# Kernel optimization log

Hardware: AMD Instinct MI355X
Metric: run time of the kernel (lower is better)

## Reference

```python
import jax, jax.numpy as jnp
import numpy as np

B, D, H = 32768, 688, 4
DH = D // H          # 172 head dim (d_model // h, overrides ctor d_k)
MH = 128             # mlp hidden
EPS = 1e-5
SCALE = 1.0 / float(np.sqrt(DH))


def _ln(x, g, b):
    m = jnp.mean(x, -1, keepdims=True)
    v = jnp.var(x, -1, keepdims=True)  # biased var, matches torch LayerNorm
    return (x - m) / jnp.sqrt(v + EPS) * g + b


def setup_inputs() -> dict:
    key = jax.random.key(0)
    ks = jax.random.split(key, 16)
    w = lambda k, o, i: jax.random.normal(k, (o, i), jnp.float32) * 0.001  # init.normal_(std=0.001)
    z = lambda n: jnp.zeros((n,), jnp.float32)
    o = lambda n: jnp.ones((n,), jnp.float32)
    return dict(
        x=jax.random.normal(ks[0], (B, D), jnp.float32),
        x2=jax.random.normal(ks[1], (B, D), jnp.float32),
        Wq_v=w(ks[2], D, D), bq_v=z(D),
        Wk_v=w(ks[3], D, D), bk_v=z(D),
        Wv_v=w(ks[4], D, D), bv_v=z(D),
        Wq_i=w(ks[5], D, D), bq_i=z(D),
        Wk_i=w(ks[6], D, D), bk_i=z(D),
        Wv_i=w(ks[7], D, D), bv_i=z(D),
        Wo_v=w(ks[8], D, D), bo_v=z(D),
        Wo_i=w(ks[9], D, D), bo_i=z(D),
        ln1_g=o(D), ln1_b=z(D), ln2_g=o(D), ln2_b=z(D),
        ln3_g=o(D), ln3_b=z(D), ln4_g=o(D), ln4_b=z(D),
        m1v_W=w(ks[10], MH, D), m1v_b=z(MH),
        m2v_W=w(ks[11], D, MH), m2v_b=z(D),
        m1i_W=w(ks[12], MH, D), m1i_b=z(MH),
        m2i_W=w(ks[13], D, MH), m2i_b=z(D),
        coef=o(8),  # LearnableCoefficient 1..8, all init to 1.0
    )


def reference(x, x2,
              Wq_v, bq_v, Wk_v, bk_v, Wv_v, bv_v,
              Wq_i, bq_i, Wk_i, bk_i, Wv_i, bv_i,
              Wo_v, bo_v, Wo_i, bo_i,
              ln1_g, ln1_b, ln2_g, ln2_b, ln3_g, ln3_b, ln4_g, ln4_b,
              m1v_W, m1v_b, m2v_W, m2v_b, m1i_W, m1i_b, m2i_W, m2i_b,
              coef):
    rgb = _ln(x, ln1_g, ln1_b)
    ir = _ln(x2, ln2_g, ln2_b)
    proj = lambda t, W, b: (t @ W.T + b).reshape(-1, H, DH)  # (B, h, d_k)
    q_vis, k_vis, v_vis = proj(rgb, Wq_v, bq_v), proj(rgb, Wk_v, bk_v), proj(rgb, Wv_v, bv_v)
    q_ir, k_ir, v_ir = proj(ir, Wq_i, bq_i), proj(ir, Wk_i, bk_i), proj(ir, Wv_i, bv_i)
    # cross attention over heads: scores are (B, h, h)
    att_vis = jax.nn.softmax(jnp.einsum('bhd,bgd->bhg', q_ir, k_vis) * SCALE, -1)
    att_ir = jax.nn.softmax(jnp.einsum('bhd,bgd->bhg', q_vis, k_ir) * SCALE, -1)
    out_vis = jnp.einsum('bhg,bgd->bhd', att_vis, v_vis).reshape(-1, D) @ Wo_v.T + bo_v
    out_ir = jnp.einsum('bhg,bgd->bhd', att_ir, v_ir).reshape(-1, D) @ Wo_i.T + bo_i
    out_vis = coef[0] * x + coef[1] * out_vis
    out_ir = coef[2] * x2 + coef[3] * out_ir
    mv = jax.nn.gelu(_ln(out_vis, ln3_g, ln3_b) @ m1v_W.T + m1v_b, approximate=False) @ m2v_W.T + m2v_b
    mi = jax.nn.gelu(_ln(out_ir, ln4_g, ln4_b) @ m1i_W.T + m1i_b, approximate=False) @ m2i_W.T + m2i_b
    out_vis = coef[4] * out_vis + coef[5] * mv
    out_ir = coef[6] * out_ir + coef[7] * mi
    return out_vis, out_ir
```

## Files before the change

### kernel.cpp

```cpp
#include <hip/hip_runtime.h>
#include <cmath>


#define B_ROWS 32768
#define D_DIM  688
#define DP     704
#define DH_DIM 172
#define MH_DIM 128

typedef unsigned short ushort_t;
typedef __attribute__((ext_vector_type(8))) __bf16 bf16x8;
typedef __attribute__((ext_vector_type(4))) float  f32x4;

__device__ __forceinline__ float b2f(ushort_t u) {
    return __builtin_bit_cast(float, (unsigned int)u << 16);
}
__device__ __forceinline__ ushort_t f2bf(float f) {
    unsigned int u = __builtin_bit_cast(unsigned int, f);
    u += 0x7FFFu + ((u >> 16) & 1u);
    return (ushort_t)(u >> 16);
}

__device__ __forceinline__ void gl2lds16(const ushort_t* g, ushort_t* l) {
    __builtin_amdgcn_global_load_lds(
        (const __attribute__((address_space(1))) unsigned int*)g,
        (__attribute__((address_space(3))) unsigned int*)l, 16, 0, 0);
}

struct CvtJobs {
    const float* src[12];
    ushort_t*    dst[12];
    int O[12], Opad[12], Kin[12], Kpad[12];
    int bstart[13];
};

__global__ __launch_bounds__(256)
void cvt_all(CvtJobs jobs)
{
    int b = blockIdx.x;
    int j = 0;
    while (b >= jobs.bstart[j + 1]) ++j;
    const int t = (b - jobs.bstart[j]) * 256 + threadIdx.x;
    const int Kpad = jobs.Kpad[j];
    const int Kin  = jobs.Kin[j];
    const int cpr  = Kpad >> 3;
    if (t >= jobs.Opad[j] * cpr) return;
    const int o = t / cpr;
    const int c = t - o * cpr;
    unsigned int p0 = 0, p1 = 0, p2 = 0, p3 = 0;
    if (o < jobs.O[j] && (c * 8 + 8) <= Kin) {
        const float* s = jobs.src[j] + (size_t)o * Kin + c * 8;
        float4 f0 = reinterpret_cast<const float4*>(s)[0];
        float4 f1 = reinterpret_cast<const float4*>(s)[1];
        p0 = f2bf(f0.x) | ((unsigned int)f2bf(f0.y) << 16);
        p1 = f2bf(f0.z) | ((unsigned int)f2bf(f0.w) << 16);
        p2 = f2bf(f1.x) | ((unsigned int)f2bf(f1.y) << 16);
        p3 = f2bf(f1.z) | ((unsigned int)f2bf(f1.w) << 16);
    }
    *reinterpret_cast<uint4*>(jobs.dst[j] + (size_t)o * Kpad + c * 8) =
        make_uint4(p0, p1, p2, p3);
}

__global__ __launch_bounds__(256)
void pack_bias(const float* __restrict__ a0, const float* __restrict__ a1,
               const float* __restrict__ a2, const float* __restrict__ b0,
               const float* __restrict__ b1, const float* __restrict__ b2,
               float* __restrict__ dv, float* __restrict__ di)
{
    int t = blockIdx.x * 256 + threadIdx.x;
    if (t >= 2064) return;
    float v, w;
    if (t < 688)       { v = a0[t];        w = b0[t]; }
    else if (t < 1376) { v = a1[t - 688];  w = b1[t - 688]; }
    else               { v = a2[t - 1376]; w = b2[t - 1376]; }
    dv[t] = v; di[t] = w;
}

__global__ __launch_bounds__(256)
void ln_kernel(const float* __restrict__ Xv, const float* __restrict__ Xi,
               const float* __restrict__ gv, const float* __restrict__ bv,
               const float* __restrict__ gi, const float* __restrict__ bi,
               ushort_t* __restrict__ Yv, ushort_t* __restrict__ Yi)
{
    const int lane = threadIdx.x & 63;
    const int wave = threadIdx.x >> 6;
    const long w = (long)blockIdx.x * 4 + wave;
    const float* X; const float* g; const float* b; ushort_t* Y; long r;
    if (w < B_ROWS) { X = Xv; g = gv; b = bv; Y = Yv; r = w; }
    else            { X = Xi; g = gi; b = bi; Y = Yi; r = w - B_ROWS; }

    const float4* row = reinterpret_cast<const float4*>(X + r * D_DIM);
    float4 v0 = row[lane];
    float4 v1 = row[lane + 64];
    float4 v2 = make_float4(0.f, 0.f, 0.f, 0.f);
    if (lane < 44) v2 = row[lane + 128];

    float s  = v0.x + v0.y + v0.z + v0.w + v1.x + v1.y + v1.z + v1.w
             + v2.x + v2.y + v2.z + v2.w;
    float s2 = v0.x*v0.x + v0.y*v0.y + v0.z*v0.z + v0.w*v0.w
             + v1.x*v1.x + v1.y*v1.y + v1.z*v1.z + v1.w*v1.w
             + v2.x*v2.x + v2.y*v2.y + v2.z*v2.z + v2.w*v2.w;
#pragma unroll
    for (int m = 32; m; m >>= 1) { s += __shfl_xor(s, m); s2 += __shfl_xor(s2, m); }

    const float mean = s * (1.f / 688.f);
    const float var  = s2 * (1.f / 688.f) - mean * mean;
    const float rstd = rsqrtf(var + 1e-5f);

    const float4* g4 = reinterpret_cast<const float4*>(g);
    const float4* b4 = reinterpret_cast<const float4*>(b);
    ushort4* out4 = reinterpret_cast<ushort4*>(Y + r * DP);

    {
        float4 gg = g4[lane], bb = b4[lane];
        ushort4 o;
        o.x = f2bf((v0.x - mean) * rstd * gg.x + bb.x);
        o.y = f2bf((v0.y - mean) * rstd * gg.y + bb.y);
        o.z = f2bf((v0.z - mean) * rstd * gg.z + bb.z);
        o.w = f2bf((v0.w - mean) * rstd * gg.w + bb.w);
        out4[lane] = o;
    }
    {
        float4 gg = g4[lane + 64], bb = b4[lane + 64];
        ushort4 o;
        o.x = f2bf((v1.x - mean) * rstd * gg.x + bb.x);
        o.y = f2bf((v1.y - mean) * rstd * gg.y + bb.y);
        o.z = f2bf((v1.z - mean) * rstd * gg.z + bb.z);
        o.w = f2bf((v1.w - mean) * rstd * gg.w + bb.w);
        out4[lane + 64] = o;
    }
    if (lane < 44) {
        float4 gg = g4[lane + 128], bb = b4[lane + 128];
        ushort4 o;
        o.x = f2bf((v2.x - mean) * rstd * gg.x + bb.x);
        o.y = f2bf((v2.y - mean) * rstd * gg.y + bb.y);
        o.z = f2bf((v2.z - mean) * rstd * gg.z + bb.z);
        o.w = f2bf((v2.w - mean) * rstd * gg.w + bb.w);
        out4[lane + 128] = o;
    } else if (lane < 48) {
        out4[lane + 128] = make_ushort4(0, 0, 0, 0);
    }
}

template<int MODE>
__global__ __launch_bounds__(512, 1)
void gemm8(const ushort_t* __restrict__ A0, const ushort_t* __restrict__ A1,
           const ushort_t* __restrict__ W0, const ushort_t* __restrict__ W1,
           const float* __restrict__ bias0, const float* __restrict__ bias1,
           ushort_t* __restrict__ out0, ushort_t* __restrict__ out1,
           const float* __restrict__ res0, const float* __restrict__ res1,
           const float* __restrict__ coef, int ca0, int cb0, int ca1, int cb1,
           int NBn, int N, int K, int lda, int ldw, int ldo)
{
    __shared__ __align__(16) ushort_t lds8[65536];

    const int q8 = gridDim.x >> 3;
    const int v  = (blockIdx.x & 7) * q8 + (blockIdx.x >> 3);
    const int nb = v % NBn;
    const int tmp = v / NBn;
    const int mb = tmp & 127;
    const int zz = tmp >> 7;

    const ushort_t* A = zz ? A1 : A0;
    const ushort_t* W = zz ? W1 : W0;
    const float* bias = zz ? bias1 : bias0;
    ushort_t* outp    = zz ? out1 : out0;
    const float* resid = zz ? res1 : res0;
    const int ca = zz ? ca1 : ca0;
    const int cb = zz ? cb1 : cb0;

    const int tid  = threadIdx.x;
    const int lane = tid & 63;
    const int wave = tid >> 6;
    const int wrow = wave >> 2;
    const int wcol = wave & 3;
    const int m0 = mb * 256;
    const int n0 = nb * 256;
    const int rl16 = lane & 15;
    const int q4   = lane >> 4;

    const int r0 = tid >> 3;
    const int u0 = tid & 7;
    const int swz0 = ((u0 ^ (r0 & 7)) * 8);

    f32x4 acc[8][4];
#pragma unroll
    for (int i = 0; i < 8; ++i)
#pragma unroll
        for (int j = 0; j < 4; ++j)
            acc[i][j] = f32x4{0.f, 0.f, 0.f, 0.f};

    const int NT = K >> 6;

#define STAGE8(mat, rbase, ld, kt, hf, tilebase) do {                              \
    const ushort_t* _s = (mat) + (size_t)((rbase) + (hf)*128 + r0) * (ld)          \
                         + (kt)*64 + swz0;                                         \
    gl2lds16(_s,                 (tilebase) + (hf)*8192 + wave*512);               \
    gl2lds16(_s + 64*(size_t)(ld), (tilebase) + (hf)*8192 + 4096 + wave*512);      \
} while (0)

#define RD_A(base, mib, kkv) do {                                                  \
    _Pragma("unroll")                                                              \
    for (int i = 0; i < 4; ++i) {                                                  \
        const int row_ = wrow*128 + ((mib)+i)*16 + rl16;                           \
        const int un_  = (((kkv) >> 3) + q4) ^ (lane & 7);                         \
        af[i] = *reinterpret_cast<const bf16x8*>((base) + row_*64 + un_*8);        \
    } } while (0)

#define RD_B(base, kkv) do {                                                       \
    _Pragma("unroll")                                                              \
    for (int j = 0; j < 4; ++j) {                                                  \
        const int row_ = wcol*64 + j*16 + rl16;                                    \
        const int un_  = (((kkv) >> 3) + q4) ^ (lane & 7);                         \
        bw[j] = *reinterpret_cast<const bf16x8*>((base) + row_*64 + un_*8);        \
    } } while (0)

#define MFMA16(mib) do {                                                           \
    __builtin_amdgcn_s_setprio(1);                                                 \
    _Pragma("unroll")                                                              \
    for (int i = 0; i < 4; ++i)                                                    \
    _Pragma("unroll")                                                              \
    for (int j = 0; j < 4; ++j)                                                    \
        acc[(mib)+i][j] =                                                          \
            __builtin_amdgcn_mfma_f32_16x16x32_bf16(af[i], bw[j], acc[(mib)+i][j], \
                                                    0, 0, 0);                      \
    __builtin_amdgcn_s_setprio(0);                                                 \
} while (0)

    STAGE8(A, m0, lda, 0, 0, lds8);
    STAGE8(A, m0, lda, 0, 1, lds8);
    STAGE8(W, n0, ldw, 0, 0, lds8 + 32768);
    STAGE8(W, n0, ldw, 0, 1, lds8 + 32768);
    STAGE8(W, n0, ldw, 1, 0, lds8 + 49152);
    asm volatile("s_waitcnt vmcnt(2)" ::: "memory");
    __builtin_amdgcn_s_barrier();

    for (int t = 0; t < NT; ++t) {
        ushort_t* const Ab  = lds8 + ((t & 1) * 16384);
        ushort_t* const Bb  = lds8 + 32768 + ((t & 1) * 16384);
        ushort_t* const An  = lds8 + (((t + 1) & 1) * 16384);
        ushort_t* const Bn1 = lds8 + 32768 + (((t + 1) & 1) * 16384);
        ushort_t* const Bn2 = Bb;
        const int tn1 = (t + 1 < NT) ? t + 1 : NT - 1;
        const int tn2 = (t + 2 < NT) ? t + 2 : NT - 1;

        bf16x8 af[4], bw[4];

        RD_A(Ab, 0, 0);
        RD_B(Bb, 0);
        STAGE8(A, m0, lda, tn1, 0, An);
        STAGE8(W, n0, ldw, tn1, 1, Bn1);
        __builtin_amdgcn_s_barrier();
        MFMA16(0);
        __builtin_amdgcn_s_barrier();

        RD_A(Ab, 4, 0);
        STAGE8(A, m0, lda, tn1, 1, An);
        __builtin_amdgcn_s_barrier();
        MFMA16(4);
        __builtin_amdgcn_s_barrier();

        RD_A(Ab, 0, 32);
        RD_B(Bb, 32);
        __builtin_amdgcn_s_barrier();
        MFMA16(0);
        __builtin_amdgcn_s_barrier();

        RD_A(Ab, 4, 32);
        STAGE8(W, n0, ldw, tn2, 0, Bn2);
        asm volatile("s_waitcnt vmcnt(2)" ::: "memory");
        __builtin_amdgcn_s_barrier();
        MFMA16(4);
        __builtin_amdgcn_s_barrier();
    }

    asm volatile("s_waitcnt vmcnt(0)" ::: "memory");
    __builtin_amdgcn_s_barrier();

    ushort_t* const Cl = lds8;
#pragma unroll
    for (int mi = 0; mi < 8; ++mi)
#pragma unroll
        for (int nj = 0; nj < 4; ++nj)
#pragma unroll
            for (int r = 0; r < 4; ++r) {
                const int row  = wrow*128 + mi*16 + q4*4 + r;
                const int colL = wcol*64 + nj*16 + rl16;
                const int blk  = (colL >> 3) ^ (((row >> 2) & 3) << 1);
                Cl[row*256 + blk*8 + (colL & 7)] = f2bf(acc[mi][nj][r]);
            }
    __syncthreads();

    float cA = 0.f, cB = 1.f;
    if constexpr (MODE == 1) { cA = coef[ca]; cB = coef[cb]; }
#pragma unroll
    for (int it2 = 0; it2 < 16; ++it2) {
        const int c   = it2 * 512 + tid;
        const int row = c >> 5;
        const int lb  = c & 31;
        const int gcol = n0 + lb * 8;
        if (gcol >= N) continue;
        const int pb = lb ^ (((row >> 2) & 3) << 1);
        uint4 pv = *reinterpret_cast<const uint4*>(Cl + row*256 + pb*8);
        const ushort_t* pu = (const ushort_t*)&pv;
        float4 b0 = *reinterpret_cast<const float4*>(bias + gcol);
        float4 b1 = *reinterpret_cast<const float4*>(bias + gcol + 4);
        const float bb[8] = {b0.x, b0.y, b0.z, b0.w, b1.x, b1.y, b1.z, b1.w};
        const size_t idx = (size_t)(m0 + row) * ldo + gcol;
        ushort_t o[8];
        if constexpr (MODE == 0) {
#pragma unroll
            for (int k = 0; k < 8; ++k) o[k] = f2bf(b2f(pu[k]) + bb[k]);
        } else {
            const float* rp = resid + idx;
            float4 r0_ = reinterpret_cast<const float4*>(rp)[0];
            float4 r1_ = reinterpret_cast<const float4*>(rp)[1];
            const float rr[8] = {r0_.x, r0_.y, r0_.z, r0_.w, r1_.x, r1_.y, r1_.z, r1_.w};
#pragma unroll
            for (int k = 0; k < 8; ++k)
                o[k] = f2bf(cA * rr[k] + cB * (b2f(pu[k]) + bb[k]));
        }
        *reinterpret_cast<uint4*>(outp + idx) = *reinterpret_cast<uint4*>(o);
    }
#undef STAGE8
#undef RD_A
#undef RD_B
#undef MFMA16
}

template<int MODE>
__global__ __launch_bounds__(256, 4)
void gemm2(const ushort_t* __restrict__ A0, const ushort_t* __restrict__ A1,
           const ushort_t* __restrict__ W0, const ushort_t* __restrict__ W1,
           const float* __restrict__ bias0, const float* __restrict__ bias1,
           void* __restrict__ out0, void* __restrict__ out1,
           const void* __restrict__ res0, const void* __restrict__ res1,
           const float* __restrict__ coef,
           int ca0, int cb0, int ca1, int cb1,
           int NBn, int N, int K, int lda, int ldw, int ldo)
{
    __shared__ __align__(16) ushort_t smem[16384];
    ushort_t* As = smem;
    ushort_t* Bs = smem + 8192;

    const int q  = gridDim.x >> 3;
    const int vb = (blockIdx.x & 7) * q + (blockIdx.x >> 3);
    const int nb = vb % NBn;
    const int tmp = vb / NBn;
    const int mb = tmp & 255;
    const int zz = tmp >> 8;

    const ushort_t* A = zz ? A1 : A0;
    const ushort_t* W = zz ? W1 : W0;
    const float* bias = zz ? bias1 : bias0;
    void* outp        = zz ? out1 : out0;
    const void* resid = zz ? res1 : res0;
    const int ca = zz ? ca1 : ca0;
    const int cb = zz ? cb1 : cb0;

    const int tid  = threadIdx.x;
    const int lane = tid & 63;
    const int wave = tid >> 6;
    const int m0 = mb * 128;
    const int n0 = nb * 128;
    const int wm = (wave >> 1) * 64;
    const int wn = (wave & 1) * 64;

    const int s0 = wave * 128 + lane;
    const int s1 = s0 + 64;
    const ushort_t* pa0 = A + (size_t)(m0 + (s0 >> 2)) * lda + (s0 & 3) * 8;
    const ushort_t* pa1 = A + (size_t)(m0 + (s1 >> 2)) * lda + (s1 & 3) * 8;
    const ushort_t* pb0 = W + (size_t)(n0 + (s0 >> 2)) * ldw + (s0 & 3) * 8;
    const ushort_t* pb1 = W + (size_t)(n0 + (s1 >> 2)) * ldw + (s1 & 3) * 8;

    f32x4 acc[4][4];
#pragma unroll
    for (int i = 0; i < 4; ++i)
#pragma unroll
        for (int j = 0; j < 4; ++j)
            acc[i][j] = f32x4{0.f, 0.f, 0.f, 0.f};

    const int ko = (lane >> 4) * 8;
    const int rl = lane & 15;
    const int nkt = K / 32;

    auto stage = [&](int buf, int kt) {
        const int kof = kt * 32;
        ushort_t* ad = As + buf * 4096 + wave * 1024;
        ushort_t* bd = Bs + buf * 4096 + wave * 1024;
        gl2lds16(pa0 + kof, ad);
        gl2lds16(pa1 + kof, ad + 512);
        gl2lds16(pb0 + kof, bd);
        gl2lds16(pb1 + kof, bd + 512);
    };

    stage(0, 0);
    __syncthreads();

    for (int kt = 0; kt < nkt; ++kt) {
        const int cur = kt & 1;
        if (kt + 1 < nkt) stage(cur ^ 1, kt + 1);

        const ushort_t* Ab = As + cur * 4096;
        const ushort_t* Bb = Bs + cur * 4096;
        bf16x8 af[4], bwv[4];
#pragma unroll
        for (int i = 0; i < 4; ++i) {
            af[i]  = *reinterpret_cast<const bf16x8*>(&Ab[(wm + i * 16 + rl) * 32 + ko]);
            bwv[i] = *reinterpret_cast<const bf16x8*>(&Bb[(wn + i * 16 + rl) * 32 + ko]);
        }
#pragma unroll
        for (int i = 0; i < 4; ++i)
#pragma unroll
            for (int j = 0; j < 4; ++j)
                acc[i][j] = __builtin_amdgcn_mfma_f32_16x16x32_bf16(af[i], bwv[j], acc[i][j], 0, 0, 0);
        __syncthreads();
    }

    float cA = 0.f, cB = 1.f;
    if constexpr (MODE == 3) { cA = coef[ca]; cB = coef[cb]; }
    const int rb = (lane >> 4) * 4;
    const int cl = lane & 15;
    ushort_t* C = smem;
#pragma unroll
    for (int j = 0; j < 4; ++j) {
        const int lcol = wn + j * 16 + cl;
        const int col = n0 + lcol;
        const float bc = (col < N) ? bias[col] : 0.f;
#pragma unroll
        for (int i = 0; i < 4; ++i) {
            const int lrow = wm + i * 16 + rb;
#pragma unroll
            for (int r = 0; r < 4; ++r) {
                float val = acc[i][j][r] + bc;
                C[(lrow + r) * 128 + lcol] = f2bf(val);
            }
        }
    }
    __syncthreads();

#pragma unroll
    for (int p = 0; p < 8; ++p) {
        const int c = tid + p * 256;
        const int lrow = c >> 4;
        const int lcl = (c & 15) * 8;
        const int gcol = n0 + lcl;
        if (gcol >= N) continue;
        const size_t idx = (size_t)(m0 + lrow) * ldo + gcol;
        uint4 pv = *reinterpret_cast<const uint4*>(&C[lrow * 128 + lcl]);
        uint4 rv = *reinterpret_cast<const uint4*>((const ushort_t*)resid + idx);
        const ushort_t* pu = (const ushort_t*)&pv;
        const ushort_t* ru = (const ushort_t*)&rv;
        float o[8];
#pragma unroll
        for (int k = 0; k < 8; ++k)
            o[k] = cA * b2f(ru[k]) + cB * b2f(pu[k]);
        float4* op = reinterpret_cast<float4*>((float*)outp + idx);
        op[0] = make_float4(o[0], o[1], o[2], o[3]);
        op[1] = make_float4(o[4], o[5], o[6], o[7]);
    }
}

__global__ __launch_bounds__(256)
void lnmlp1(const ushort_t* __restrict__ ov0, const ushort_t* __restrict__ ov1,
            const float* __restrict__ g0, const float* __restrict__ b0,
            const float* __restrict__ g1, const float* __restrict__ b1,
            const ushort_t* __restrict__ W10, const ushort_t* __restrict__ W11,
            const float* __restrict__ mb0, const float* __restrict__ mb1,
            ushort_t* __restrict__ out0, ushort_t* __restrict__ out1)
{
    __shared__ __align__(16) ushort_t hraw[64 * 712];
    __shared__ float glds[704];
    __shared__ float blds[704];
    __shared__ float mlds[64];
    __shared__ float rlds[64];

    const int zz = blockIdx.y;
    const ushort_t* ovb = zz ? ov1 : ov0;
    const float* lg = zz ? g1 : g0;
    const float* lb = zz ? b1 : b0;
    const ushort_t* W1 = zz ? W11 : W10;
    const float* mbias = zz ? mb1 : mb0;
    ushort_t* outp = zz ? out1 : out0;

    const int tid  = threadIdx.x;
    const int lane = tid & 63;
    const int wv   = tid >> 6;
    const long r0  = (long)blockIdx.x * 64;

    if (tid < 176) {
        float4 gg = make_float4(0, 0, 0, 0), bb = make_float4(0, 0, 0, 0);
        if (tid < 172) {
            gg = reinterpret_cast<const float4*>(lg)[tid];
            bb = reinterpret_cast<const float4*>(lb)[tid];
        }
        reinterpret_cast<float4*>(glds)[tid] = gg;
        reinterpret_cast<float4*>(blds)[tid] = bb;
    }

#pragma unroll
    for (int it = 0; it < 22; ++it) {
        const int c = it * 256 + tid;
        const int row = c / 88;
        const int u = c - row * 88;
        uint4 vv = make_uint4(0, 0, 0, 0);
        if (u < 86)
            vv = *reinterpret_cast<const uint4*>(ovb + (r0 + row) * 688 + u * 8);
        *reinterpret_cast<uint4*>(&hraw[row * 712 + u * 8]) = vv;
    }
    __syncthreads();

    for (int rr = 0; rr < 16; ++rr) {
        const int row = wv * 16 + rr;
        const ushort_t* hp = &hraw[row * 712];
        ushort4 a0 = *reinterpret_cast<const ushort4*>(hp + lane * 4);
        ushort4 a1 = *reinterpret_cast<const ushort4*>(hp + 256 + lane * 4);
        ushort4 a2 = make_ushort4(0, 0, 0, 0);
        if (lane < 44) a2 = *reinterpret_cast<const ushort4*>(hp + 512 + lane * 4);
        float e[12] = {b2f(a0.x), b2f(a0.y), b2f(a0.z), b2f(a0.w),
                       b2f(a1.x), b2f(a1.y), b2f(a1.z), b2f(a1.w),
                       b2f(a2.x), b2f(a2.y), b2f(a2.z), b2f(a2.w)};
        float s = 0.f, s2 = 0.f;
#pragma unroll
        for (int k = 0; k < 12; ++k) { s += e[k]; s2 += e[k] * e[k]; }
#pragma unroll
        for (int m = 32; m; m >>= 1) { s += __shfl_xor(s, m); s2 += __shfl_xor(s2, m); }
        if (lane == 0) {
            const float mean = s * (1.f / 688.f);
            const float var  = s2 * (1.f / 688.f) - mean * mean;
            mlds[row] = mean;
            rlds[row] = rsqrtf(var + 1e-5f);
        }
    }
    __syncthreads();

#pragma unroll
    for (int it = 0; it < 22; ++it) {
        const int c = it * 256 + tid;
        if (c < 5504) {
            const int row = c / 86;
            const int u = c - row * 86;
            uint4 vv = *reinterpret_cast<const uint4*>(&hraw[row * 712 + u * 8]);
            const float mean = mlds[row], rstd = rlds[row];
            const ushort_t* pe = (const ushort_t*)&vv;
            ushort_t o[8];
#pragma unroll
            for (int k = 0; k < 8; ++k)
                o[k] = f2bf((b2f(pe[k]) - mean) * rstd * glds[u * 8 + k] + blds[u * 8 + k]);
            *reinterpret_cast<uint4*>(&hraw[row * 712 + u * 8]) = *reinterpret_cast<uint4*>(o);
        }
    }
    __syncthreads();

    const int rl16 = lane & 15;
    const int q4   = lane >> 4;
    f32x4 acc[4][2];
#pragma unroll
    for (int i = 0; i < 4; ++i) { acc[i][0] = f32x4{0,0,0,0}; acc[i][1] = f32x4{0,0,0,0}; }

    for (int kt = 0; kt < 11; ++kt) {
#pragma unroll
        for (int kk = 0; kk < 64; kk += 32) {
            bf16x8 af[4], bw[2];
#pragma unroll
            for (int n = 0; n < 2; ++n)
                bw[n] = *reinterpret_cast<const bf16x8*>(
                    W1 + (size_t)(wv * 32 + n * 16 + rl16) * 704 + kt * 64 + kk + q4 * 8);
#pragma unroll
            for (int i = 0; i < 4; ++i)
                af[i] = *reinterpret_cast<const bf16x8*>(
                    &hraw[(i * 16 + rl16) * 712 + kt * 64 + kk + q4 * 8]);
#pragma unroll
            for (int i = 0; i < 4; ++i)
#pragma unroll
                for (int n = 0; n < 2; ++n)
                    acc[i][n] = __builtin_amdgcn_mfma_f32_16x16x32_bf16(
                        af[i], bw[n], acc[i][n], 0, 0, 0);
        }
    }

    const int rb = q4 * 4;
#pragma unroll
    for (int n = 0; n < 2; ++n) {
        const int col = wv * 32 + n * 16 + rl16;
        const float bc = mbias[col];
#pragma unroll
        for (int i = 0; i < 4; ++i)
#pragma unroll
            for (int r = 0; r < 4; ++r) {
                float val = acc[i][n][r] + bc;
                val = 0.5f * val * (1.0f + erff(val * 0.70710678118654752f));
                outp[(r0 + i * 16 + rb + r) * 128 + col] = f2bf(val);
            }
    }
}

__global__ __launch_bounds__(256)
void attn_kernel(const ushort_t* __restrict__ qkv_v, const ushort_t* __restrict__ qkv_i,
                 ushort_t* __restrict__ ctx_v, ushort_t* __restrict__ ctx_i)
{
    const int lane = threadIdx.x & 63;
    const int wave = threadIdx.x >> 6;
    const long r = (long)blockIdx.x * 4 + wave;
    const ushort_t* bv = qkv_v + r * 2064;
    const ushort_t* bi = qkv_i + r * 2064;

    float sv[4][4], si[4][4];
#pragma unroll
    for (int h = 0; h < 4; ++h)
#pragma unroll
        for (int g = 0; g < 4; ++g) { sv[h][g] = 0.f; si[h][g] = 0.f; }

    float vvr[3][4], vir[3][4];
#pragma unroll
    for (int it = 0; it < 3; ++it) {
        const int d = lane + it * 64;
        const bool ok = d < DH_DIM;
        float qv[4], kv[4], qi[4], ki[4];
#pragma unroll
        for (int h = 0; h < 4; ++h) {
            const int o = h * DH_DIM + d;
            qv[h]      = ok ? b2f(bv[o]) : 0.f;
            kv[h]      = ok ? b2f(bv[D_DIM + o]) : 0.f;
            vvr[it][h] = ok ? b2f(bv[2 * D_DIM + o]) : 0.f;
            qi[h]      = ok ? b2f(bi[o]) : 0.f;
            ki[h]      = ok ? b2f(bi[D_DIM + o]) : 0.f;
            vir[it][h] = ok ? b2f(bi[2 * D_DIM + o]) : 0.f;
        }
#pragma unroll
        for (int h = 0; h < 4; ++h)
#pragma unroll
            for (int g = 0; g < 4; ++g) {
                sv[h][g] += qi[h] * kv[g];
                si[h][g] += qv[h] * ki[g];
            }
    }

#pragma unroll
    for (int h = 0; h < 4; ++h)
#pragma unroll
        for (int g = 0; g < 4; ++g) {
            float a = sv[h][g], b = si[h][g];
#pragma unroll
            for (int m = 32; m; m >>= 1) { a += __shfl_xor(a, m); b += __shfl_xor(b, m); }
            sv[h][g] = a; si[h][g] = b;
        }

    const float scale = 0.07624928516630235f;
    float av[4][4], ai[4][4];
#pragma unroll
    for (int h = 0; h < 4; ++h) {
        float m1 = fmaxf(fmaxf(sv[h][0], sv[h][1]), fmaxf(sv[h][2], sv[h][3])) * scale;
        float m2 = fmaxf(fmaxf(si[h][0], si[h][1]), fmaxf(si[h][2], si[h][3])) * scale;
        float d1 = 0.f, d2 = 0.f;
#pragma unroll
        for (int g = 0; g < 4; ++g) {
            av[h][g] = expf(sv[h][g] * scale - m1); d1 += av[h][g];
            ai[h][g] = expf(si[h][g] * scale - m2); d2 += ai[h][g];
        }
        const float r1 = 1.f / d1, r2 = 1.f / d2;
#pragma unroll
        for (int g = 0; g < 4; ++g) { av[h][g] *= r1; ai[h][g] *= r2; }
    }

#pragma unroll
    for (int it = 0; it < 3; ++it) {
        const int d = lane + it * 64;
        if (d < DH_DIM) {
#pragma unroll
            for (int h = 0; h < 4; ++h) {
                float cv = av[h][0] * vvr[it][0] + av[h][1] * vvr[it][1]
                         + av[h][2] * vvr[it][2] + av[h][3] * vvr[it][3];
                float ci = ai[h][0] * vir[it][0] + ai[h][1] * vir[it][1]
                         + ai[h][2] * vir[it][2] + ai[h][3] * vir[it][3];
                ctx_v[r * DP + h * DH_DIM + d] = f2bf(cv);
                ctx_i[r * DP + h * DH_DIM + d] = f2bf(ci);
            }
        }
    }
    if (lane < 16) {
        ctx_v[r * DP + 688 + lane] = 0;
        ctx_i[r * DP + 688 + lane] = 0;
    }
}

extern "C" void kernel_launch(void* const* d_in, const int* in_sizes, int n_in,
                              void* d_out, int out_size, void* d_ws, size_t ws_size,
                              hipStream_t stream)
{
    if (n_in < 35) return;
    const float* x     = (const float*)d_in[0];
    const float* x2    = (const float*)d_in[1];
    const float* Wq_v  = (const float*)d_in[2];
    const float* bq_v  = (const float*)d_in[3];
    const float* Wk_v  = (const float*)d_in[4];
    const float* bk_v  = (const float*)d_in[5];
    const float* Wv_v  = (const float*)d_in[6];
    const float* bv_v  = (const float*)d_in[7];
    const float* Wq_i  = (const float*)d_in[8];
    const float* bq_i  = (const float*)d_in[9];
    const float* Wk_i  = (const float*)d_in[10];
    const float* bk_i  = (const float*)d_in[11];
    const float* Wv_i  = (const float*)d_in[12];
    const float* bv_i  = (const float*)d_in[13];
    const float* Wo_v  = (const float*)d_in[14];
    const float* bo_v  = (const float*)d_in[15];
    const float* Wo_i  = (const float*)d_in[16];
    const float* bo_i  = (const float*)d_in[17];
    const float* ln1_g = (const float*)d_in[18];
    const float* ln1_b = (const float*)d_in[19];
    const float* ln2_g = (const float*)d_in[20];
    const float* ln2_b = (const float*)d_in[21];
    const float* ln3_g = (const float*)d_in[22];
    const float* ln3_b = (const float*)d_in[23];
    const float* ln4_g = (const float*)d_in[24];
    const float* ln4_b = (const float*)d_in[25];
    const float* m1v_W = (const float*)d_in[26];
    const float* m1v_b = (const float*)d_in[27];
    const float* m2v_W = (const float*)d_in[28];
    const float* m2v_b = (const float*)d_in[29];
    const float* m1i_W = (const float*)d_in[30];
    const float* m1i_b = (const float*)d_in[31];
    const float* m2i_W = (const float*)d_in[32];
    const float* m2i_b = (const float*)d_in[33];
    const float* coef  = (const float*)d_in[34];

    const size_t BDP = (size_t)B_ROWS * DP;
    const size_t BD  = (size_t)B_ROWS * D_DIM;

    char* ws = (char*)d_ws;
    size_t off = 0;
    auto give = [&](size_t bytes) {
        char* p = ws + off;
        off += (bytes + 255) & ~(size_t)255;
        return p;
    };
    ushort_t* Wcat_v = (ushort_t*)give(2304ull * DP * 2);
    ushort_t* Wcat_i = (ushort_t*)give(2304ull * DP * 2);
    ushort_t* Wo_vb  = (ushort_t*)give(768ull * DP * 2);
    ushort_t* Wo_ib  = (ushort_t*)give(768ull * DP * 2);
    ushort_t* m1vb   = (ushort_t*)give(128ull * DP * 2);
    ushort_t* m1ib   = (ushort_t*)give(128ull * DP * 2);
    ushort_t* m2vb   = (ushort_t*)give(768ull * 128 * 2);
    ushort_t* m2ib   = (ushort_t*)give(768ull * 128 * 2);
    float*    bcat_v = (float*)give(2064 * 4);
    float*    bcat_i = (float*)give(2064 * 4);
    char* regX = give(BDP * 2 * 2);
    char* regQ = give((size_t)B_ROWS * 2064 * 2 * 2);
    char* regG = give((size_t)B_ROWS * MH_DIM * 2 * 2);
    if (ws_size < off) return;

    ushort_t* xn_v  = (ushort_t*)regX;
    ushort_t* xn_i  = xn_v + BDP;
    ushort_t* ctx_v = xn_v;
    ushort_t* ctx_i = xn_i;
    ushort_t* qkv_v = (ushort_t*)regQ;
    ushort_t* qkv_i = qkv_v + (size_t)B_ROWS * 2064;
    ushort_t* ovb   = (ushort_t*)regQ;
    ushort_t* oib   = ovb + BD;
    ushort_t* g_v   = (ushort_t*)regG;
    ushort_t* g_i   = g_v + (size_t)B_ROWS * MH_DIM;

    float* ov = (float*)d_out;
    float* oi = ov + BD;

    CvtJobs J;
    const float* srcs[12] = {Wq_v, Wk_v, Wv_v, Wq_i, Wk_i, Wv_i,
                             Wo_v, Wo_i, m1v_W, m1i_W, m2v_W, m2i_W};
    ushort_t* dsts[12] = {Wcat_v, Wcat_v + 688 * DP, Wcat_v + 1376 * DP,
                          Wcat_i, Wcat_i + 688 * DP, Wcat_i + 1376 * DP,
                          Wo_vb, Wo_ib, m1vb, m1ib, m2vb, m2ib};
    int Os[12]    = {688, 688, 688, 688, 688, 688, 688, 688, 128, 128, 688, 688};
    int Opads[12] = {688, 688, 928, 688, 688, 928, 768, 768, 128, 128, 768, 768};
    int Kins[12]  = {688, 688, 688, 688, 688, 688, 688, 688, 688, 688, 128, 128};
    int Kpads[12] = {DP, DP, DP, DP, DP, DP, DP, DP, DP, DP, 128, 128};
    int bs = 0;
    for (int j = 0; j < 12; ++j) {
        J.src[j] = srcs[j]; J.dst[j] = dsts[j];
        J.O[j] = Os[j]; J.Opad[j] = Opads[j]; J.Kin[j] = Kins[j]; J.Kpad[j] = Kpads[j];
        J.bstart[j] = bs;
        bs += (Opads[j] * (Kpads[j] >> 3) + 255) / 256;
    }
    J.bstart[12] = bs;
    cvt_all<<<dim3(bs), dim3(256), 0, stream>>>(J);

    pack_bias<<<dim3(9), dim3(256), 0, stream>>>(bq_v, bk_v, bv_v, bq_i, bk_i, bv_i,
                                                 bcat_v, bcat_i);

    ln_kernel<<<dim3(2 * B_ROWS / 4), dim3(256), 0, stream>>>(
        x, x2, ln1_g, ln1_b, ln2_g, ln2_b, xn_v, xn_i);

    gemm8<0><<<dim3(128 * 9 * 2), dim3(512), 0, stream>>>(
        xn_v, xn_i, Wcat_v, Wcat_i, bcat_v, bcat_i, qkv_v, qkv_i,
        nullptr, nullptr, nullptr, 0, 0, 0, 0, 9, 2064, DP, DP, DP, 2064);

    attn_kernel<<<dim3(B_ROWS / 4), dim3(256), 0, stream>>>(qkv_v, qkv_i, ctx_v, ctx_i);

    gemm8<1><<<dim3(128 * 3 * 2), dim3(512), 0, stream>>>(
        ctx_v, ctx_i, Wo_vb, Wo_ib, bo_v, bo_i, ovb, oib,
        x, x2, coef, 0, 1, 2, 3, 3, 688, DP, DP, DP, 688);

    lnmlp1<<<dim3(B_ROWS / 64, 2), dim3(256), 0, stream>>>(
        ovb, oib, ln3_g, ln3_b, ln4_g, ln4_b, m1vb, m1ib, m1v_b, m1i_b, g_v, g_i);

    gemm2<3><<<dim3(256 * 6 * 2), dim3(256), 0, stream>>>(
        g_v, g_i, m2vb, m2ib, m2v_b, m2i_b, ov, oi,
        ovb, oib, coef, 4, 5, 6, 7, 6, 688, 128, 128, 128, 688);
}
```

Baseline: 707.7 us.

## Fuse LayerNorm, MLP up-projection, GELU and down-projection into one kernel

Merges the lnmlp1 kernel and the second MLP GEMM into a single mlp_fused kernel that handles 32 rows per block. The GELU activations stay in shared memory, and the down-projection runs directly from there with the bias and residual combine applied in the epilogue. This removes the global-memory round trip of the hidden activations and one kernel launch. In exchange, W1 and W2 are re-read from global or cache by every block, and the output stores are scalar and strided rather than vectorised.

```diff
diff --git a/kernel.cpp b/kernel.cpp
--- a/kernel.cpp
+++ b/kernel.cpp
@@ -328,165 +328,40 @@
 #undef MFMA16
 }
 
-template<int MODE>
-__global__ __launch_bounds__(256, 4)
-void gemm2(const ushort_t* __restrict__ A0, const ushort_t* __restrict__ A1,
-           const ushort_t* __restrict__ W0, const ushort_t* __restrict__ W1,
-           const float* __restrict__ bias0, const float* __restrict__ bias1,
-           void* __restrict__ out0, void* __restrict__ out1,
-           const void* __restrict__ res0, const void* __restrict__ res1,
-           const float* __restrict__ coef,
-           int ca0, int cb0, int ca1, int cb1,
-           int NBn, int N, int K, int lda, int ldw, int ldo)
+__global__ __launch_bounds__(256)
+void mlp_fused(const ushort_t* __restrict__ ov0, const ushort_t* __restrict__ ov1,
+               const float* __restrict__ g0, const float* __restrict__ b0,
+               const float* __restrict__ g1, const float* __restrict__ b1,
+               const ushort_t* __restrict__ W10, const ushort_t* __restrict__ W11,
+               const float* __restrict__ mb10, const float* __restrict__ mb11,
+               const ushort_t* __restrict__ W20, const ushort_t* __restrict__ W21,
+               const float* __restrict__ mb20, const float* __restrict__ mb21,
+               const float* __restrict__ coef,
+               float* __restrict__ out0, float* __restrict__ out1)
 {
-    __shared__ __align__(16) ushort_t smem[16384];
-    ushort_t* As = smem;
-    ushort_t* Bs = smem + 8192;
-
-    const int q  = gridDim.x >> 3;
-    const int vb = (blockIdx.x & 7) * q + (blockIdx.x >> 3);
-    const int nb = vb % NBn;
-    const int tmp = vb / NBn;
-    const int mb = tmp & 255;
-    const int zz = tmp >> 8;
-
-    const ushort_t* A = zz ? A1 : A0;
-    const ushort_t* W = zz ? W1 : W0;
-    const float* bias = zz ? bias1 : bias0;
-    void* outp        = zz ? out1 : out0;
-    const void* resid = zz ? res1 : res0;
-    const int ca = zz ? ca1 : ca0;
-    const int cb = zz ? cb1 : cb0;
-
-    const int tid  = threadIdx.x;
-    const int lane = tid & 63;
-    const int wave = tid >> 6;
-    const int m0 = mb * 128;
-    const int n0 = nb * 128;
-    const int wm = (wave >> 1) * 64;
-    const int wn = (wave & 1) * 64;
-
-    const int s0 = wave * 128 + lane;
-    const int s1 = s0 + 64;
-    const ushort_t* pa0 = A + (size_t)(m0 + (s0 >> 2)) * lda + (s0 & 3) * 8;
-    const ushort_t* pa1 = A + (size_t)(m0 + (s1 >> 2)) * lda + (s1 & 3) * 8;
-    const ushort_t* pb0 = W + (size_t)(n0 + (s0 >> 2)) * ldw + (s0 & 3) * 8;
-    const ushort_t* pb1 = W + (size_t)(n0 + (s1 >> 2)) * ldw + (s1 & 3) * 8;
-
-    f32x4 acc[4][4];
-#pragma unroll
-    for (int i = 0; i < 4; ++i)
-#pragma unroll
-        for (int j = 0; j < 4; ++j)
-            acc[i][j] = f32x4{0.f, 0.f, 0.f, 0.f};
-
-    const int ko = (lane >> 4) * 8;
-    const int rl = lane & 15;
-    const int nkt = K / 32;
-
-    auto stage = [&](int buf, int kt) {
-        const int kof = kt * 32;
-        ushort_t* ad = As + buf * 4096 + wave * 1024;
-        ushort_t* bd = Bs + buf * 4096 + wave * 1024;
-        gl2lds16(pa0 + kof, ad);
-        gl2lds16(pa1 + kof, ad + 512);
-        gl2lds16(pb0 + kof, bd);
-        gl2lds16(pb1 + kof, bd + 512);
-    };
-
-    stage(0, 0);
-    __syncthreads();
-
-    for (int kt = 0; kt < nkt; ++kt) {
-        const int cur = kt & 1;
-        if (kt + 1 < nkt) stage(cur ^ 1, kt + 1);
-
-        const ushort_t* Ab = As + cur * 4096;
-        const ushort_t* Bb = Bs + cur * 4096;
-        bf16x8 af[4], bwv[4];
-#pragma unroll
-        for (int i = 0; i < 4; ++i) {
-            af[i]  = *reinterpret_cast<const bf16x8*>(&Ab[(wm + i * 16 + rl) * 32 + ko]);
-            bwv[i] = *reinterpret_cast<const bf16x8*>(&Bb[(wn + i * 16 + rl) * 32 + ko]);
-        }
-#pragma unroll
-        for (int i = 0; i < 4; ++i)
-#pragma unroll
-            for (int j = 0; j < 4; ++j)
-                acc[i][j] = __builtin_amdgcn_mfma_f32_16x16x32_bf16(af[i], bwv[j], acc[i][j], 0, 0, 0);
-        __syncthreads();
-    }
-
-    float cA = 0.f, cB = 1.f;
-    if constexpr (MODE == 3) { cA = coef[ca]; cB = coef[cb]; }
-    const int rb = (lane >> 4) * 4;
-    const int cl = lane & 15;
-    ushort_t* C = smem;
-#pragma unroll
-    for (int j = 0; j < 4; ++j) {
-        const int lcol = wn + j * 16 + cl;
-        const int col = n0 + lcol;
-        const float bc = (col < N) ? bias[col] : 0.f;
-#pragma unroll
-        for (int i = 0; i < 4; ++i) {
-            const int lrow = wm + i * 16 + rb;
-#pragma unroll
-            for (int r = 0; r < 4; ++r) {
-                float val = acc[i][j][r] + bc;
-                C[(lrow + r) * 128 + lcol] = f2bf(val);
-            }
-        }
-    }
-    __syncthreads();
-
-#pragma unroll
-    for (int p = 0; p < 8; ++p) {
-        const int c = tid + p * 256;
-        const int lrow = c >> 4;
-        const int lcl = (c & 15) * 8;
-        const int gcol = n0 + lcl;
-        if (gcol >= N) continue;
-        const size_t idx = (size_t)(m0 + lrow) * ldo + gcol;
-        uint4 pv = *reinterpret_cast<const uint4*>(&C[lrow * 128 + lcl]);
-        uint4 rv = *reinterpret_cast<const uint4*>((const ushort_t*)resid + idx);
-        const ushort_t* pu = (const ushort_t*)&pv;
-        const ushort_t* ru = (const ushort_t*)&rv;
-        float o[8];
-#pragma unroll
-        for (int k = 0; k < 8; ++k)
-            o[k] = cA * b2f(ru[k]) + cB * b2f(pu[k]);
-        float4* op = reinterpret_cast<float4*>((float*)outp + idx);
-        op[0] = make_float4(o[0], o[1], o[2], o[3]);
-        op[1] = make_float4(o[4], o[5], o[6], o[7]);
-    }
-}
-
-__global__ __launch_bounds__(256)
-void lnmlp1(const ushort_t* __restrict__ ov0, const ushort_t* __restrict__ ov1,
-            const float* __restrict__ g0, const float* __restrict__ b0,
-            const float* __restrict__ g1, const float* __restrict__ b1,
-            const ushort_t* __restrict__ W10, const ushort_t* __restrict__ W11,
-            const float* __restrict__ mb0, const float* __restrict__ mb1,
-            ushort_t* __restrict__ out0, ushort_t* __restrict__ out1)
-{
-    __shared__ __align__(16) ushort_t hraw[64 * 712];
+    __shared__ __align__(16) ushort_t hraw[32 * 712];
+    __shared__ __align__(16) ushort_t gbuf[32 * 136];
     __shared__ float glds[704];
     __shared__ float blds[704];
-    __shared__ float mlds[64];
-    __shared__ float rlds[64];
+    __shared__ float mlds[32];
+    __shared__ float rlds[32];
 
     const int zz = blockIdx.y;
     const ushort_t* ovb = zz ? ov1 : ov0;
     const float* lg = zz ? g1 : g0;
     const float* lb = zz ? b1 : b0;
     const ushort_t* W1 = zz ? W11 : W10;
-    const float* mbias = zz ? mb1 : mb0;
-    ushort_t* outp = zz ? out1 : out0;
+    const float* mb1 = zz ? mb11 : mb10;
+    const ushort_t* W2 = zz ? W21 : W20;
+    const float* mb2 = zz ? mb21 : mb20;
+    float* outp = zz ? out1 : out0;
+    const float cA = coef[zz ? 6 : 4];
+    const float cB = coef[zz ? 7 : 5];
 
     const int tid  = threadIdx.x;
     const int lane = tid & 63;
     const int wv   = tid >> 6;
-    const long r0  = (long)blockIdx.x * 64;
+    const long r0  = (long)blockIdx.x * 32;
 
     if (tid < 176) {
         float4 gg = make_float4(0, 0, 0, 0), bb = make_float4(0, 0, 0, 0);
@@ -499,7 +374,7 @@
     }
 
 #pragma unroll
-    for (int it = 0; it < 22; ++it) {
+    for (int it = 0; it < 11; ++it) {
         const int c = it * 256 + tid;
         const int row = c / 88;
         const int u = c - row * 88;
@@ -510,8 +385,8 @@
     }
     __syncthreads();
 
-    for (int rr = 0; rr < 16; ++rr) {
-        const int row = wv * 16 + rr;
+    for (int rr = 0; rr < 8; ++rr) {
+        const int row = wv * 8 + rr;
         const ushort_t* hp = &hraw[row * 712];
         ushort4 a0 = *reinterpret_cast<const ushort4*>(hp + lane * 4);
         ushort4 a1 = *reinterpret_cast<const ushort4*>(hp + 256 + lane * 4);
@@ -535,9 +410,9 @@
     __syncthreads();
 
 #pragma unroll
-    for (int it = 0; it < 22; ++it) {
+    for (int it = 0; it < 11; ++it) {
         const int c = it * 256 + tid;
-        if (c < 5504) {
+        if (c < 2752) {
             const int row = c / 86;
             const int u = c - row * 86;
             uint4 vv = *reinterpret_cast<const uint4*>(&hraw[row * 712 + u * 8]);
@@ -554,43 +429,76 @@
 
     const int rl16 = lane & 15;
     const int q4   = lane >> 4;
-    f32x4 acc[4][2];
-#pragma unroll
-    for (int i = 0; i < 4; ++i) { acc[i][0] = f32x4{0,0,0,0}; acc[i][1] = f32x4{0,0,0,0}; }
-
-    for (int kt = 0; kt < 11; ++kt) {
-#pragma unroll
-        for (int kk = 0; kk < 64; kk += 32) {
-            bf16x8 af[4], bw[2];
-#pragma unroll
-            for (int n = 0; n < 2; ++n)
-                bw[n] = *reinterpret_cast<const bf16x8*>(
-                    W1 + (size_t)(wv * 32 + n * 16 + rl16) * 704 + kt * 64 + kk + q4 * 8);
-#pragma unroll
-            for (int i = 0; i < 4; ++i)
-                af[i] = *reinterpret_cast<const bf16x8*>(
-                    &hraw[(i * 16 + rl16) * 712 + kt * 64 + kk + q4 * 8]);
-#pragma unroll
-            for (int i = 0; i < 4; ++i)
+
+    {
+        f32x4 acc[2][2];
+#pragma unroll
+        for (int i = 0; i < 2; ++i) { acc[i][0] = f32x4{0,0,0,0}; acc[i][1] = f32x4{0,0,0,0}; }
+        for (int kt = 0; kt < 11; ++kt) {
+#pragma unroll
+            for (int kk = 0; kk < 64; kk += 32) {
+                bf16x8 af[2], bw[2];
 #pragma unroll
                 for (int n = 0; n < 2; ++n)
-                    acc[i][n] = __builtin_amdgcn_mfma_f32_16x16x32_bf16(
-                        af[i], bw[n], acc[i][n], 0, 0, 0);
-        }
-    }
-
-    const int rb = q4 * 4;
-#pragma unroll
-    for (int n = 0; n < 2; ++n) {
-        const int col = wv * 32 + n * 16 + rl16;
-        const float bc = mbias[col];
-#pragma unroll
-        for (int i = 0; i < 4; ++i)
+                    bw[n] = *reinterpret_cast<const bf16x8*>(
+                        W1 + (size_t)(wv * 32 + n * 16 + rl16) * 704 + kt * 64 + kk + q4 * 8);
+#pragma unroll
+                for (int i = 0; i < 2; ++i)
+                    af[i] = *reinterpret_cast<const bf16x8*>(
+                        &hraw[(i * 16 + rl16) * 712 + kt * 64 + kk + q4 * 8]);
+#pragma unroll
+                for (int i = 0; i < 2; ++i)
+#pragma unroll
+                    for (int n = 0; n < 2; ++n)
+                        acc[i][n] = __builtin_amdgcn_mfma_f32_16x16x32_bf16(
+                            af[i], bw[n], acc[i][n], 0, 0, 0);
+            }
+        }
+        const int rb = q4 * 4;
+#pragma unroll
+        for (int n = 0; n < 2; ++n) {
+            const int col = wv * 32 + n * 16 + rl16;
+            const float bc = mb1[col];
+#pragma unroll
+            for (int i = 0; i < 2; ++i)
+#pragma unroll
+                for (int r = 0; r < 4; ++r) {
+                    float val = acc[i][n][r] + bc;
+                    val = 0.5f * val * (1.0f + erff(val * 0.70710678118654752f));
+                    gbuf[(i * 16 + rb + r) * 136 + col] = f2bf(val);
+                }
+        }
+    }
+    __syncthreads();
+
+    for (int ch = 0; ch < 11; ++ch) {
+        const int col16 = wv * 176 + ch * 16;
+        if (col16 >= 688) continue;
+        f32x4 acc2[2];
+        acc2[0] = f32x4{0, 0, 0, 0};
+        acc2[1] = f32x4{0, 0, 0, 0};
+#pragma unroll
+        for (int kk = 0; kk < 4; ++kk) {
+            bf16x8 bw2 = *reinterpret_cast<const bf16x8*>(
+                W2 + (size_t)(col16 + rl16) * 128 + kk * 32 + q4 * 8);
+            bf16x8 af2[2];
+#pragma unroll
+            for (int i = 0; i < 2; ++i)
+                af2[i] = *reinterpret_cast<const bf16x8*>(
+                    &gbuf[(i * 16 + rl16) * 136 + kk * 32 + q4 * 8]);
+#pragma unroll
+            for (int i = 0; i < 2; ++i)
+                acc2[i] = __builtin_amdgcn_mfma_f32_16x16x32_bf16(af2[i], bw2, acc2[i], 0, 0, 0);
+        }
+        const int col = col16 + rl16;
+        const float bc = mb2[col];
+#pragma unroll
+        for (int i = 0; i < 2; ++i)
 #pragma unroll
             for (int r = 0; r < 4; ++r) {
-                float val = acc[i][n][r] + bc;
-                val = 0.5f * val * (1.0f + erff(val * 0.70710678118654752f));
-                outp[(r0 + i * 16 + rb + r) * 128 + col] = f2bf(val);
+                const long row = r0 + i * 16 + q4 * 4 + r;
+                const float raw = b2f(ovb[row * 688 + col]);
+                outp[row * 688 + col] = cA * raw + cB * (acc2[i][r] + bc);
             }
     }
 }
@@ -747,7 +655,6 @@
     float*    bcat_i = (float*)give(2064 * 4);
     char* regX = give(BDP * 2 * 2);
     char* regQ = give((size_t)B_ROWS * 2064 * 2 * 2);
-    char* regG = give((size_t)B_ROWS * MH_DIM * 2 * 2);
     if (ws_size < off) return;
 
     ushort_t* xn_v  = (ushort_t*)regX;
@@ -758,8 +665,6 @@
     ushort_t* qkv_i = qkv_v + (size_t)B_ROWS * 2064;
     ushort_t* ovb   = (ushort_t*)regQ;
     ushort_t* oib   = ovb + BD;
-    ushort_t* g_v   = (ushort_t*)regG;
-    ushort_t* g_i   = g_v + (size_t)B_ROWS * MH_DIM;
 
     float* ov = (float*)d_out;
     float* oi = ov + BD;
@@ -800,10 +705,8 @@
         ctx_v, ctx_i, Wo_vb, Wo_ib, bo_v, bo_i, ovb, oib,
         x, x2, coef, 0, 1, 2, 3, 3, 688, DP, DP, DP, 688);
 
-    lnmlp1<<<dim3(B_ROWS / 64, 2), dim3(256), 0, stream>>>(
-        ovb, oib, ln3_g, ln3_b, ln4_g, ln4_b, m1vb, m1ib, m1v_b, m1i_b, g_v, g_i);
-
-    gemm2<3><<<dim3(256 * 6 * 2), dim3(256), 0, stream>>>(
-        g_v, g_i, m2vb, m2ib, m2v_b, m2i_b, ov, oi,
-        ovb, oib, coef, 4, 5, 6, 7, 6, 688, 128, 128, 128, 688);
-}
+    mlp_fused<<<dim3(B_ROWS / 32, 2), dim3(256), 0, stream>>>(
+        ovb, oib, ln3_g, ln3_b, ln4_g, ln4_b,
+        m1vb, m1ib, m1v_b, m1i_b, m2vb, m2ib, m2v_b, m2i_b,
+        coef, ov, oi);
+}
```

Result: faster. 681.6 us (-3.7%).
